# Kernel optimization log

Measured on AMD Instinct MI355X. Metric: run time of the kernel, lower is better.

Reference implementation:

```python
import jax, jax.numpy as jnp
import numpy as np

T, B = 200, 4096
CONTEXT_FRAMES = 6


def _lstm_cell(x, h, c, wih, whh, bih, bhh):
    # PyTorch LSTM gate order: i, f, g, o
    g = x @ wih.T + bih + h @ whh.T + bhh
    i, f, gg, o = jnp.split(g, 4, axis=-1)
    c2 = jax.nn.sigmoid(f) * c + jax.nn.sigmoid(i) * jnp.tanh(gg)
    h2 = jax.nn.sigmoid(o) * jnp.tanh(c2)
    return h2, c2


def _ff(x, w1, b1, w2, b2):
    return jax.nn.relu(jax.nn.relu(x @ w1.T + b1) @ w2.T + b2)


def setup_inputs() -> dict:
    key = jax.random.key(0)
    ks = iter(jax.random.split(key, 48))

    def p(shape, scale=0.1):
        return (jax.random.normal(next(ks), shape) * scale).astype(jnp.float32)

    inp = {
        'tactiles': p((T, B, 48), 1.0),
        'actions': p((T, B, 3), 1.0),
        'context': p((T, B, 48), 1.0),
    }
    # LSTM params: (4H, in), (4H, H), (4H,), (4H,)
    for name, din, h in [('l1', 48, 48), ('l2', 96, 96), ('l3', 144, 144), ('l4', 48, 48)]:
        inp[name + '_wih'] = p((4 * h, din))
        inp[name + '_whh'] = p((4 * h, h))
        inp[name + '_bih'] = p((4 * h,))
        inp[name + '_bhh'] = p((4 * h,))
    # Feedforward params
    for name, din, hid, dout in [('f1', 6, 48, 48), ('f2', 144, 144, 96), ('f3', 96, 96, 48)]:
        inp[name + '_w1'] = p((hid, din))
        inp[name + '_b1'] = p((hid,))
        inp[name + '_w2'] = p((dout, hid))
        inp[name + '_b2'] = p((dout,))
    # Hidden-state inits (original uses torch.rand -> uniform[0,1))
    for name, h in [('1', 48), ('2', 96), ('3', 144), ('4', 48)]:
        inp['h0_' + name] = jax.random.uniform(next(ks), (B, h), dtype=jnp.float32)
        inp['c0_' + name] = jax.random.uniform(next(ks), (B, h), dtype=jnp.float32)
    return inp


def reference(tactiles, actions, context,
              l1_wih, l1_whh, l1_bih, l1_bhh,
              l2_wih, l2_whh, l2_bih, l2_bhh,
              l3_wih, l3_whh, l3_bih, l3_bhh,
              l4_wih, l4_whh, l4_bih, l4_bhh,
              f1_w1, f1_b1, f1_w2, f1_b2,
              f2_w1, f2_b1, f2_w2, f2_b2,
              f3_w1, f3_b1, f3_w2, f3_b2,
              h0_1, c0_1, h0_2, c0_2, h0_3, c0_3, h0_4, c0_4):
    state = actions[0]  # [B, 3], fixed across time

    def step(carry, inp):
        h1, c1, h2, c2, h3, c3, h4, c4, out6 = carry
        tac, act, ctx, t = inp
        x1 = jnp.where(t > CONTEXT_FRAMES - 1, out6, tac)  # [B, 48]
        h1, c1 = _lstm_cell(x1, h1, c1, l1_wih, l1_whh, l1_bih, l1_bhh)
        x2 = jnp.concatenate([ctx, h1], axis=1)  # [B, 96]
        h2, c2 = _lstm_cell(x2, h2, c2, l2_wih, l2_whh, l2_bih, l2_bhh)
        sa = jnp.concatenate([state, act], axis=1)  # [B, 6]
        sa_out = _ff(sa, f1_w1, f1_b1, f1_w2, f1_b2)  # [B, 48]
        x3 = jnp.concatenate([sa_out, h2], axis=1)  # [B, 144]
        h3, c3 = _lstm_cell(x3, h3, c3, l3_wih, l3_whh, l3_bih, l3_bhh)
        out4 = _ff(h3, f2_w1, f2_b1, f2_w2, f2_b2)  # [B, 96]
        out5 = _ff(out4, f3_w1, f3_b1, f3_w2, f3_b2)  # [B, 48]
        h4, c4 = _lstm_cell(out5, h4, c4, l4_wih, l4_whh, l4_bih, l4_bhh)
        return (h1, c1, h2, c2, h3, c3, h4, c4, h4), h4

    carry0 = (h0_1, c0_1, h0_2, c0_2, h0_3, c0_3, h0_4, c0_4, jnp.zeros_like(h0_1))
    ts = jnp.arange(tactiles.shape[0])
    _, outs = jax.lax.scan(step, carry0, (tactiles, actions, context, ts))
    return outs  # [T, B, 48]
```

## Files before the change

kernel.cpp:

```cpp
#include <hip/hip_runtime.h>
#include <math.h>


#define NT 256
#define MROWS 8
#define TSTEPS 200
#define BATCH 4096
#define XS 10
#define GS 9

#define L1W   0
#define L1B   18432
#define L2W   18624
#define L2B   92352
#define L3W   92736
#define L3B   258624
#define L4W   259200
#define L4B   277632
#define F1AW  277824
#define F1AB  278208
#define F1BW  278256
#define F1BB  280560
#define F2AW  280608
#define F2AB  301344
#define F2BW  301488
#define F2BB  315312
#define F3AW  315408
#define F3AB  324624
#define F3BW  324720
#define F3BB  329328

#define P_GB   0
#define P_SAT  5184
#define P_F1H  5264
#define P_F2H  0
#define P_O4T  1440
#define P_F3H  2400
#define P_OUT5 3360
#define P_L4G  0
#define POOLSZ 5744

__device__ __forceinline__ float sigf(float x) { return 1.0f / (1.0f + __expf(-x)); }

__global__ void prep_lstm(const float* __restrict__ wih, const float* __restrict__ whh,
                          const float* __restrict__ bih, const float* __restrict__ bhh,
                          float* __restrict__ W, float* __restrict__ bias,
                          int Din, int H) {
    int K = Din + H;
    int N = 4 * H;
    int total = N * K;
    for (int idx = blockIdx.x * blockDim.x + threadIdx.x; idx < total + N;
         idx += gridDim.x * blockDim.x) {
        if (idx < total) {
            int c = idx / K;
            int k = idx - c * K;
            W[idx] = (k < Din) ? wih[c * Din + k] : whh[c * H + (k - Din)];
        } else {
            int c = idx - total;
            bias[c] = bih[c] + bhh[c];
        }
    }
}

__global__ void prep_ff(const float* __restrict__ w, const float* __restrict__ b,
                        float* __restrict__ W, float* __restrict__ bias,
                        int K, int Kpad, int N) {
    int total = N * Kpad;
    for (int idx = blockIdx.x * blockDim.x + threadIdx.x; idx < total + N;
         idx += gridDim.x * blockDim.x) {
        if (idx < total) {
            int c = idx / Kpad;
            int k = idx - c * Kpad;
            W[idx] = (k < K) ? w[c * K + k] : 0.0f;
        } else {
            int c = idx - total;
            bias[c] = b[c];
        }
    }
}

template <int TC, int ROWS, bool RELU>
__device__ __forceinline__ void mm(
    const float* __restrict__ w0, const float* __restrict__ w1,
    const float* __restrict__ w2,
    float b0, float b1, float b2,
    const float* __restrict__ x0, int K0,
    const float* __restrict__ x1, int K1,
    const float* __restrict__ x2, int K2,
    int rbase,
    float* __restrict__ g0, float* __restrict__ g1, float* __restrict__ g2) {
    float a0[ROWS], a1[ROWS], a2[ROWS];
#pragma unroll
    for (int r = 0; r < ROWS; ++r) { a0[r] = 0.f; a1[r] = 0.f; a2[r] = 0.f; }
    int ko = 0;
#pragma unroll
    for (int s = 0; s < 3; ++s) {
        const float* xb = (s == 0) ? x0 : (s == 1) ? x1 : x2;
        int K = (s == 0) ? K0 : (s == 1) ? K1 : K2;
        if (K > 0) {
            const float* xp = xb + rbase;
#pragma unroll 2
            for (int k = 0; k < K; k += 4) {
                float4 wv0 = *(const float4*)(w0 + ko + k);
                float4 wv1 = (TC > 1) ? *(const float4*)(w1 + ko + k) : wv0;
                float4 wv2 = (TC > 2) ? *(const float4*)(w2 + ko + k) : wv0;
                const float* f0 = (const float*)&wv0;
                const float* f1p = (const float*)&wv1;
                const float* f2p = (const float*)&wv2;
#pragma unroll
                for (int q = 0; q < 4; ++q) {
                    const float* xq = xp + (k + q) * XS;
#pragma unroll
                    for (int rr = 0; rr < ROWS; rr += 2) {
                        float2 xv = *(const float2*)(xq + rr);
                        a0[rr]     = fmaf(xv.x, f0[q], a0[rr]);
                        a0[rr + 1] = fmaf(xv.y, f0[q], a0[rr + 1]);
                        if (TC > 1) {
                            a1[rr]     = fmaf(xv.x, f1p[q], a1[rr]);
                            a1[rr + 1] = fmaf(xv.y, f1p[q], a1[rr + 1]);
                        }
                        if (TC > 2) {
                            a2[rr]     = fmaf(xv.x, f2p[q], a2[rr]);
                            a2[rr + 1] = fmaf(xv.y, f2p[q], a2[rr + 1]);
                        }
                    }
                }
            }
            ko += K;
        }
    }
#pragma unroll
    for (int r = 0; r < ROWS; ++r) {
        float v0 = a0[r] + b0;
        if (RELU) v0 = fmaxf(v0, 0.f);
        g0[r] = v0;
        if (TC > 1) {
            float v1 = a1[r] + b1;
            if (RELU) v1 = fmaxf(v1, 0.f);
            g1[r] = v1;
        }
        if (TC > 2) {
            float v2 = a2[r] + b2;
            if (RELU) v2 = fmaxf(v2, 0.f);
            g2[r] = v2;
        }
    }
}

template <int H, int R, int NCS>
__device__ __forceinline__ void lstm_epi(const float* __restrict__ gb, int gs,
                                         float* __restrict__ hT,
                                         float (&cs)[NCS], int idx0, int stride) {
    const int E = H * R;
#pragma unroll
    for (int n = 0; n < NCS; ++n) {
        int idx = idx0 + n * stride;
        if (idx < E) {
            int r = idx & (R - 1);
            int j = idx / R;
            float gi = gb[j * gs + r];
            float gf = gb[(j + H) * gs + r];
            float gg = gb[(j + 2 * H) * gs + r];
            float go = gb[(j + 3 * H) * gs + r];
            float c2 = sigf(gf) * cs[n] + sigf(gi) * tanhf(gg);
            cs[n] = c2;
            hT[j * XS + r] = sigf(go) * tanhf(c2);
        }
    }
}

template <int H, int R, int NCS>
__device__ __forceinline__ void c_init(const float* __restrict__ c0, int r0,
                                       float (&cs)[NCS], int idx0, int stride) {
    const int E = H * R;
#pragma unroll
    for (int n = 0; n < NCS; ++n) {
        int idx = idx0 + n * stride;
        if (idx < E) {
            int r = idx & (R - 1);
            int j = idx / R;
            cs[n] = c0[(size_t)(r0 + r) * H + j];
        }
    }
}

__global__ __launch_bounds__(256, 2) void model_kernel(
    const float* __restrict__ tactiles, const float* __restrict__ actions,
    const float* __restrict__ context, const float* __restrict__ ws,
    const float* __restrict__ h01, const float* __restrict__ c01,
    const float* __restrict__ h02, const float* __restrict__ c02,
    const float* __restrict__ h03, const float* __restrict__ c03,
    const float* __restrict__ h04, const float* __restrict__ c04,
    float* __restrict__ out) {
    __shared__ __align__(16) float tacT[48 * XS];
    __shared__ __align__(16) float ctxT[48 * XS];
    __shared__ __align__(16) float h1T[48 * XS];
    __shared__ __align__(16) float h2T[96 * XS];
    __shared__ __align__(16) float h3T[144 * XS];
    __shared__ __align__(16) float h4T[48 * XS];
    __shared__ __align__(16) float saoT[48 * XS];
    __shared__ __align__(16) float pool[POOLSZ];

    const int tid = threadIdx.x;
    const int r0 = blockIdx.x * MROWS;

    for (int i = tid; i < 48 * 8; i += NT) {
        int r = i & 7, j = i >> 3;
        h1T[j * XS + r] = h01[(size_t)(r0 + r) * 48 + j];
        h4T[j * XS + r] = h04[(size_t)(r0 + r) * 48 + j];
    }
    for (int i = tid; i < 96 * 8; i += NT) {
        int r = i & 7, j = i >> 3;
        h2T[j * XS + r] = h02[(size_t)(r0 + r) * 96 + j];
    }
    for (int i = tid; i < 144 * 8; i += NT) {
        int r = i & 7, j = i >> 3;
        h3T[j * XS + r] = h03[(size_t)(r0 + r) * 144 + j];
    }

    float cs1[2] = {0.f, 0.f};
    float cs2[3] = {0.f, 0.f, 0.f};
    float cs3[5] = {0.f, 0.f, 0.f, 0.f, 0.f};
    float cs4[2] = {0.f, 0.f};
    if (tid >= 64) c_init<48, 8, 2>(c01, r0, cs1, tid - 64, 192);
    c_init<96, 8, 3>(c02, r0, cs2, tid, NT);
    c_init<144, 8, 5>(c03, r0, cs3, tid, NT);
    c_init<48, 8, 2>(c04, r0, cs4, tid, NT);

    float bL1  = (tid < 192) ? ws[L1B + tid] : 0.f;
    float bL2a = ws[L2B + tid];
    float bL2b = (tid < 128) ? ws[L2B + tid + 256] : 0.f;
    float bL3a = ws[L3B + tid];
    float bL3b = ws[L3B + tid + 256];
    float bL3c = (tid < 64) ? ws[L3B + tid + 512] : 0.f;
    float bL4  = (tid < 192) ? ws[L4B + tid] : 0.f;
    float bF1a = (tid >= 192 && tid < 240) ? ws[F1AB + (tid - 192)] : 0.f;
    float bF1b = (tid < 48) ? ws[F1BB + tid] : 0.f;
    float bF2a = (tid < 144) ? ws[F2AB + tid] : 0.f;
    float bF2b = (tid < 192) ? ws[F2BB + (tid % 96)] : 0.f;
    float bF3a = (tid < 192) ? ws[F3AB + (tid % 96)] : 0.f;
    float bF3b = (tid < 192) ? ws[F3BB + (tid % 48)] : 0.f;

    const int wvid = tid >> 6;
    __syncthreads();

    for (int t = 0; t < TSTEPS; ++t) {
        if (t < 6) {
            const float* src = tactiles + (size_t)t * BATCH * 48 + (size_t)r0 * 48;
            for (int i = tid; i < 96; i += NT) {
                int r = i / 12, k4 = (i % 12) * 4;
                float4 v = *(const float4*)(src + r * 48 + k4);
                tacT[(k4 + 0) * XS + r] = v.x;
                tacT[(k4 + 1) * XS + r] = v.y;
                tacT[(k4 + 2) * XS + r] = v.z;
                tacT[(k4 + 3) * XS + r] = v.w;
            }
        }
        {
            const float* src = context + (size_t)t * BATCH * 48 + (size_t)r0 * 48;
            for (int i = tid; i < 96; i += NT) {
                int r = i / 12, k4 = (i % 12) * 4;
                float4 v = *(const float4*)(src + r * 48 + k4);
                ctxT[(k4 + 0) * XS + r] = v.x;
                ctxT[(k4 + 1) * XS + r] = v.y;
                ctxT[(k4 + 2) * XS + r] = v.z;
                ctxT[(k4 + 3) * XS + r] = v.w;
            }
        }
        if (tid < 64) {
            int r = tid & 7, k = tid >> 3;
            float v = 0.f;
            if (k < 3) v = actions[(size_t)(r0 + r) * 3 + k];
            else if (k < 6) v = actions[(size_t)t * BATCH * 3 + (size_t)(r0 + r) * 3 + (k - 3)];
            pool[P_SAT + k * XS + r] = v;
        }
        __syncthreads();

        {
            const float* x1 = (t < 6) ? tacT : h4T;
            if (tid < 192)
                mm<1, 8, false>(ws + L1W + tid * 96, ws, ws, bL1, 0.f, 0.f,
                                x1, 48, h1T, 48, nullptr, 0, 0,
                                pool + P_GB + tid * GS, nullptr, nullptr);
            else if (tid < 240)
                mm<1, 8, true>(ws + F1AW + (tid - 192) * 8, ws, ws, bF1a, 0.f, 0.f,
                               pool + P_SAT, 8, nullptr, 0, nullptr, 0, 0,
                               pool + P_F1H + (tid - 192) * XS, nullptr, nullptr);
        }
        __syncthreads();

        if (tid < 48)
            mm<1, 8, true>(ws + F1BW + tid * 48, ws, ws, bF1b, 0.f, 0.f,
                           pool + P_F1H, 48, nullptr, 0, nullptr, 0, 0,
                           saoT + tid * XS, nullptr, nullptr);
        else if (tid >= 64)
            lstm_epi<48, 8, 2>(pool + P_GB, GS, h1T, cs1, tid - 64, 192);
        __syncthreads();

        if (wvid < 2)
            mm<2, 8, false>(ws + L2W + (size_t)tid * 192, ws + L2W + (size_t)(tid + 256) * 192,
                            ws, bL2a, bL2b, 0.f,
                            ctxT, 48, h1T, 48, h2T, 96, 0,
                            pool + P_GB + tid * GS, pool + P_GB + (tid + 256) * GS, nullptr);
        else
            mm<1, 8, false>(ws + L2W + (size_t)tid * 192, ws, ws, bL2a, 0.f, 0.f,
                            ctxT, 48, h1T, 48, h2T, 96, 0,
                            pool + P_GB + tid * GS, nullptr, nullptr);
        __syncthreads();
        lstm_epi<96, 8, 3>(pool + P_GB, GS, h2T, cs2, tid, NT);
        __syncthreads();

        if (wvid == 0)
            mm<3, 8, false>(ws + L3W + (size_t)tid * 288, ws + L3W + (size_t)(tid + 256) * 288,
                            ws + L3W + (size_t)(tid + 512) * 288, bL3a, bL3b, bL3c,
                            saoT, 48, h2T, 96, h3T, 144, 0,
                            pool + P_GB + tid * GS, pool + P_GB + (tid + 256) * GS,
                            pool + P_GB + (tid + 512) * GS);
        else
            mm<2, 8, false>(ws + L3W + (size_t)tid * 288, ws + L3W + (size_t)(tid + 256) * 288,
                            ws, bL3a, bL3b, 0.f,
                            saoT, 48, h2T, 96, h3T, 144, 0,
                            pool + P_GB + tid * GS, pool + P_GB + (tid + 256) * GS, nullptr);
        __syncthreads();
        lstm_epi<144, 8, 5>(pool + P_GB, GS, h3T, cs3, tid, NT);
        __syncthreads();

        if (tid < 144)
            mm<1, 8, true>(ws + F2AW + tid * 144, ws, ws, bF2a, 0.f, 0.f,
                           h3T, 144, nullptr, 0, nullptr, 0, 0,
                           pool + P_F2H + tid * XS, nullptr, nullptr);
        __syncthreads();
        if (tid < 192) {
            int c = tid % 96, rb = (tid / 96) * 4;
            mm<1, 4, true>(ws + F2BW + c * 144, ws, ws, bF2b, 0.f, 0.f,
                           pool + P_F2H, 144, nullptr, 0, nullptr, 0, rb,
                           pool + P_O4T + c * XS + rb, nullptr, nullptr);
        }
        __syncthreads();
        if (tid < 192) {
            int c = tid % 96, rb = (tid / 96) * 4;
            mm<1, 4, true>(ws + F3AW + c * 96, ws, ws, bF3a, 0.f, 0.f,
                           pool + P_O4T, 96, nullptr, 0, nullptr, 0, rb,
                           pool + P_F3H + c * XS + rb, nullptr, nullptr);
        }
        __syncthreads();
        if (tid < 192) {
            int c = tid % 48, rb = (tid / 48) * 2;
            mm<1, 2, true>(ws + F3BW + c * 96, ws, ws, bF3b, 0.f, 0.f,
                           pool + P_F3H, 96, nullptr, 0, nullptr, 0, rb,
                           pool + P_OUT5 + c * XS + rb, nullptr, nullptr);
        }
        __syncthreads();

        if (tid < 192)
            mm<1, 8, false>(ws + L4W + tid * 96, ws, ws, bL4, 0.f, 0.f,
                            pool + P_OUT5, 48, h4T, 48, nullptr, 0, 0,
                            pool + P_L4G + tid * GS, nullptr, nullptr);
        __syncthreads();
        lstm_epi<48, 8, 2>(pool + P_L4G, GS, h4T, cs4, tid, NT);
        __syncthreads();

        {
            float* dst = out + (size_t)t * BATCH * 48 + (size_t)r0 * 48;
            for (int i = tid; i < 96; i += NT) {
                int r = i / 12, j4 = (i % 12) * 4;
                float4 v;
                v.x = h4T[(j4 + 0) * XS + r];
                v.y = h4T[(j4 + 1) * XS + r];
                v.z = h4T[(j4 + 2) * XS + r];
                v.w = h4T[(j4 + 3) * XS + r];
                *(float4*)(dst + r * 48 + j4) = v;
            }
        }
    }
}

extern "C" void kernel_launch(void* const* d_in, const int* in_sizes, int n_in,
                              void* d_out, int out_size, void* d_ws, size_t ws_size,
                              hipStream_t stream) {
    const float* tac = (const float*)d_in[0];
    const float* act = (const float*)d_in[1];
    const float* ctx = (const float*)d_in[2];

    const float* l1_wih = (const float*)d_in[3];
    const float* l1_whh = (const float*)d_in[4];
    const float* l1_bih = (const float*)d_in[5];
    const float* l1_bhh = (const float*)d_in[6];
    const float* l2_wih = (const float*)d_in[7];
    const float* l2_whh = (const float*)d_in[8];
    const float* l2_bih = (const float*)d_in[9];
    const float* l2_bhh = (const float*)d_in[10];
    const float* l3_wih = (const float*)d_in[11];
    const float* l3_whh = (const float*)d_in[12];
    const float* l3_bih = (const float*)d_in[13];
    const float* l3_bhh = (const float*)d_in[14];
    const float* l4_wih = (const float*)d_in[15];
    const float* l4_whh = (const float*)d_in[16];
    const float* l4_bih = (const float*)d_in[17];
    const float* l4_bhh = (const float*)d_in[18];

    const float* f1_w1 = (const float*)d_in[19];
    const float* f1_b1 = (const float*)d_in[20];
    const float* f1_w2 = (const float*)d_in[21];
    const float* f1_b2 = (const float*)d_in[22];
    const float* f2_w1 = (const float*)d_in[23];
    const float* f2_b1 = (const float*)d_in[24];
    const float* f2_w2 = (const float*)d_in[25];
    const float* f2_b2 = (const float*)d_in[26];
    const float* f3_w1 = (const float*)d_in[27];
    const float* f3_b1 = (const float*)d_in[28];
    const float* f3_w2 = (const float*)d_in[29];
    const float* f3_b2 = (const float*)d_in[30];

    const float* h01 = (const float*)d_in[31];
    const float* c01 = (const float*)d_in[32];
    const float* h02 = (const float*)d_in[33];
    const float* c02 = (const float*)d_in[34];
    const float* h03 = (const float*)d_in[35];
    const float* c03 = (const float*)d_in[36];
    const float* h04 = (const float*)d_in[37];
    const float* c04 = (const float*)d_in[38];

    float* ws = (float*)d_ws;
    float* out = (float*)d_out;

    dim3 blk(NT);
    hipLaunchKernelGGL(prep_lstm, dim3(96), blk, 0, stream,
                       l1_wih, l1_whh, l1_bih, l1_bhh, ws + L1W, ws + L1B, 48, 48);
    hipLaunchKernelGGL(prep_lstm, dim3(256), blk, 0, stream,
                       l2_wih, l2_whh, l2_bih, l2_bhh, ws + L2W, ws + L2B, 96, 96);
    hipLaunchKernelGGL(prep_lstm, dim3(256), blk, 0, stream,
                       l3_wih, l3_whh, l3_bih, l3_bhh, ws + L3W, ws + L3B, 144, 144);
    hipLaunchKernelGGL(prep_lstm, dim3(96), blk, 0, stream,
                       l4_wih, l4_whh, l4_bih, l4_bhh, ws + L4W, ws + L4B, 48, 48);

    hipLaunchKernelGGL(prep_ff, dim3(4), blk, 0, stream,
                       f1_w1, f1_b1, ws + F1AW, ws + F1AB, 6, 8, 48);
    hipLaunchKernelGGL(prep_ff, dim3(16), blk, 0, stream,
                       f1_w2, f1_b2, ws + F1BW, ws + F1BB, 48, 48, 48);
    hipLaunchKernelGGL(prep_ff, dim3(96), blk, 0, stream,
                       f2_w1, f2_b1, ws + F2AW, ws + F2AB, 144, 144, 144);
    hipLaunchKernelGGL(prep_ff, dim3(64), blk, 0, stream,
                       f2_w2, f2_b2, ws + F2BW, ws + F2BB, 144, 144, 96);
    hipLaunchKernelGGL(prep_ff, dim3(48), blk, 0, stream,
                       f3_w1, f3_b1, ws + F3AW, ws + F3AB, 96, 96, 96);
    hipLaunchKernelGGL(prep_ff, dim3(24), blk, 0, stream,
                       f3_w2, f3_b2, ws + F3BW, ws + F3BB, 96, 96, 48);

    hipLaunchKernelGGL(model_kernel, dim3(BATCH / MROWS), blk, 0, stream,
                       tac, act, ctx, ws,
                       h01, c01, h02, c02, h03, c03, h04, c04, out);
}
```

Baseline: 17.68 ms.

## Fuse LSTM gate matmul with cell epilogue via gate-interleaved weights and double-buffered state

```diff
diff --git a/kernel.cpp b/kernel.cpp
--- a/kernel.cpp
+++ b/kernel.cpp
@@ -6,7 +6,7 @@
 #define MROWS 8
 #define TSTEPS 200
 #define BATCH 4096
-#define XS 10
+#define XS 12
 #define GS 9
 
 #define L1W   0
@@ -31,16 +31,42 @@
 #define F3BB  329328
 
 #define P_GB   0
+#define P_F2H  0
+#define P_O4T  1728
+#define P_F3H  2880
+#define P_OUT5 4032
 #define P_SAT  5184
-#define P_F1H  5264
-#define P_F2H  0
-#define P_O4T  1440
-#define P_F3H  2400
-#define P_OUT5 3360
-#define P_L4G  0
-#define POOLSZ 5744
+#define P_F1H  5280
+#define POOLSZ 5856
+
+#define H1SZ (48 * XS)
+#define H2SZ (96 * XS)
+#define H4SZ (48 * XS)
 
 __device__ __forceinline__ float sigf(float x) { return 1.0f / (1.0f + __expf(-x)); }
+
+__global__ void prep_lstm_f(const float* __restrict__ wih, const float* __restrict__ whh,
+                            const float* __restrict__ bih, const float* __restrict__ bhh,
+                            float* __restrict__ W, float* __restrict__ bias,
+                            int Din, int H) {
+    int K = Din + H;
+    int total = H * K * 4;
+    for (int idx = blockIdx.x * blockDim.x + threadIdx.x; idx < total + 4 * H;
+         idx += gridDim.x * blockDim.x) {
+        if (idx < total) {
+            int g = idx & 3;
+            int kj = idx >> 2;
+            int k = kj % K;
+            int j = kj / K;
+            int row = g * H + j;
+            W[idx] = (k < Din) ? wih[row * Din + k] : whh[row * H + (k - Din)];
+        } else {
+            int i = idx - total;
+            int g = i & 3, j = i >> 2;
+            bias[i] = bih[g * H + j] + bhh[g * H + j];
+        }
+    }
+}
 
 __global__ void prep_lstm(const float* __restrict__ wih, const float* __restrict__ whh,
                           const float* __restrict__ bih, const float* __restrict__ bhh,
@@ -79,49 +105,158 @@
     }
 }
 
-template <int TC, int ROWS, bool RELU>
-__device__ __forceinline__ void mm(
+template <int ROWS, bool EMIT>
+__device__ __forceinline__ void lstm_fused(
+    const float* __restrict__ wp, float4 bv,
+    const float* __restrict__ x0, int K0,
+    const float* __restrict__ x1, int K1,
+    const float* __restrict__ x2, int K2,
+    int rbase, float* __restrict__ hdst,
+    float (&cs)[ROWS], float* __restrict__ gout) {
+    float ai[ROWS], af[ROWS], ag[ROWS], ao[ROWS];
+#pragma unroll
+    for (int r = 0; r < ROWS; ++r) { ai[r] = af[r] = ag[r] = ao[r] = 0.f; }
+    int ko = 0;
+#pragma unroll
+    for (int s = 0; s < 3; ++s) {
+        const float* xb = (s == 0) ? x0 : (s == 1) ? x1 : x2;
+        int K = (s == 0) ? K0 : (s == 1) ? K1 : K2;
+        if (K > 0) {
+            const float* xp = xb + rbase;
+            const float* wk = wp + (size_t)ko * 4;
+#pragma unroll 4
+            for (int k = 0; k < K; ++k) {
+                float4 wv = *(const float4*)(wk + k * 4);
+                if (ROWS == 2) {
+                    float2 xv = *(const float2*)(xp + k * XS);
+                    ai[0] = fmaf(xv.x, wv.x, ai[0]); ai[1] = fmaf(xv.y, wv.x, ai[1]);
+                    af[0] = fmaf(xv.x, wv.y, af[0]); af[1] = fmaf(xv.y, wv.y, af[1]);
+                    ag[0] = fmaf(xv.x, wv.z, ag[0]); ag[1] = fmaf(xv.y, wv.z, ag[1]);
+                    ao[0] = fmaf(xv.x, wv.w, ao[0]); ao[1] = fmaf(xv.y, wv.w, ao[1]);
+                } else {
+                    float4 xv = *(const float4*)(xp + k * XS);
+                    const float* xf = (const float*)&xv;
+#pragma unroll
+                    for (int r = 0; r < ROWS; ++r) {
+                        ai[r] = fmaf(xf[r], wv.x, ai[r]);
+                        af[r] = fmaf(xf[r], wv.y, af[r]);
+                        ag[r] = fmaf(xf[r], wv.z, ag[r]);
+                        ao[r] = fmaf(xf[r], wv.w, ao[r]);
+                    }
+                }
+            }
+            ko += K;
+        }
+    }
+    float hv[ROWS];
+#pragma unroll
+    for (int r = 0; r < ROWS; ++r) {
+        float gi = sigf(ai[r] + bv.x);
+        float gf = sigf(af[r] + bv.y);
+        float gg = tanhf(ag[r] + bv.z);
+        float go = sigf(ao[r] + bv.w);
+        float c2 = gf * cs[r] + gi * gg;
+        cs[r] = c2;
+        hv[r] = go * tanhf(c2);
+    }
+    if (ROWS == 2) {
+        *(float2*)hdst = make_float2(hv[0], hv[1]);
+    } else {
+        *(float4*)hdst = make_float4(hv[0], hv[1], hv[2], hv[3]);
+    }
+    if (EMIT) {
+#pragma unroll
+        for (int r = 0; r < ROWS; ++r) gout[(size_t)r * 48] = hv[r];
+    }
+}
+
+template <int ROWS>
+__device__ __forceinline__ void ffmm(
+    const float* __restrict__ w, float b,
+    const float* __restrict__ x, int K,
+    int rbase, float* __restrict__ dst) {
+    float a[ROWS];
+#pragma unroll
+    for (int r = 0; r < ROWS; ++r) a[r] = 0.f;
+    const float* xp = x + rbase;
+#pragma unroll 2
+    for (int k = 0; k < K; k += 4) {
+        float4 wv = *(const float4*)(w + k);
+        const float* wf = (const float*)&wv;
+#pragma unroll
+        for (int q = 0; q < 4; ++q) {
+            const float* xq = xp + (k + q) * XS;
+            if (ROWS == 8) {
+                float4 u = *(const float4*)(xq);
+                float4 v = *(const float4*)(xq + 4);
+                a[0] = fmaf(u.x, wf[q], a[0]); a[1] = fmaf(u.y, wf[q], a[1]);
+                a[2] = fmaf(u.z, wf[q], a[2]); a[3] = fmaf(u.w, wf[q], a[3]);
+                a[4] = fmaf(v.x, wf[q], a[4]); a[5] = fmaf(v.y, wf[q], a[5]);
+                a[6] = fmaf(v.z, wf[q], a[6]); a[7] = fmaf(v.w, wf[q], a[7]);
+            } else if (ROWS == 4) {
+                float4 u = *(const float4*)(xq);
+                a[0] = fmaf(u.x, wf[q], a[0]); a[1] = fmaf(u.y, wf[q], a[1]);
+                a[2] = fmaf(u.z, wf[q], a[2]); a[3] = fmaf(u.w, wf[q], a[3]);
+            } else {
+                float2 u = *(const float2*)(xq);
+                a[0] = fmaf(u.x, wf[q], a[0]); a[1] = fmaf(u.y, wf[q], a[1]);
+            }
+        }
+    }
+#pragma unroll
+    for (int r = 0; r < ROWS; ++r) a[r] = fmaxf(a[r] + b, 0.f);
+    if (ROWS == 8) {
+        *(float4*)(dst) = make_float4(a[0], a[1], a[2], a[3]);
+        *(float4*)(dst + 4) = make_float4(a[4], a[5], a[6], a[7]);
+    } else if (ROWS == 4) {
+        *(float4*)(dst) = make_float4(a[0], a[1], a[2], a[3]);
+    } else {
+        *(float2*)(dst) = make_float2(a[0], a[1]);
+    }
+}
+
+template <int TC>
+__device__ __forceinline__ void l3mm(
     const float* __restrict__ w0, const float* __restrict__ w1,
     const float* __restrict__ w2,
     float b0, float b1, float b2,
     const float* __restrict__ x0, int K0,
     const float* __restrict__ x1, int K1,
     const float* __restrict__ x2, int K2,
-    int rbase,
     float* __restrict__ g0, float* __restrict__ g1, float* __restrict__ g2) {
-    float a0[ROWS], a1[ROWS], a2[ROWS];
-#pragma unroll
-    for (int r = 0; r < ROWS; ++r) { a0[r] = 0.f; a1[r] = 0.f; a2[r] = 0.f; }
+    float a0[8], a1[8], a2[8];
+#pragma unroll
+    for (int r = 0; r < 8; ++r) { a0[r] = 0.f; a1[r] = 0.f; a2[r] = 0.f; }
     int ko = 0;
 #pragma unroll
     for (int s = 0; s < 3; ++s) {
         const float* xb = (s == 0) ? x0 : (s == 1) ? x1 : x2;
         int K = (s == 0) ? K0 : (s == 1) ? K1 : K2;
         if (K > 0) {
-            const float* xp = xb + rbase;
 #pragma unroll 2
             for (int k = 0; k < K; k += 4) {
                 float4 wv0 = *(const float4*)(w0 + ko + k);
-                float4 wv1 = (TC > 1) ? *(const float4*)(w1 + ko + k) : wv0;
+                float4 wv1 = *(const float4*)(w1 + ko + k);
                 float4 wv2 = (TC > 2) ? *(const float4*)(w2 + ko + k) : wv0;
                 const float* f0 = (const float*)&wv0;
                 const float* f1p = (const float*)&wv1;
                 const float* f2p = (const float*)&wv2;
 #pragma unroll
                 for (int q = 0; q < 4; ++q) {
-                    const float* xq = xp + (k + q) * XS;
-#pragma unroll
-                    for (int rr = 0; rr < ROWS; rr += 2) {
-                        float2 xv = *(const float2*)(xq + rr);
-                        a0[rr]     = fmaf(xv.x, f0[q], a0[rr]);
-                        a0[rr + 1] = fmaf(xv.y, f0[q], a0[rr + 1]);
-                        if (TC > 1) {
-                            a1[rr]     = fmaf(xv.x, f1p[q], a1[rr]);
-                            a1[rr + 1] = fmaf(xv.y, f1p[q], a1[rr + 1]);
-                        }
+                    const float* xq = xb + (k + q) * XS;
+                    float4 u = *(const float4*)(xq);
+                    float4 v = *(const float4*)(xq + 4);
+                    const float* xf = (const float*)&u;
+                    const float* yf = (const float*)&v;
+#pragma unroll
+                    for (int r = 0; r < 4; ++r) {
+                        a0[r] = fmaf(xf[r], f0[q], a0[r]);
+                        a0[r + 4] = fmaf(yf[r], f0[q], a0[r + 4]);
+                        a1[r] = fmaf(xf[r], f1p[q], a1[r]);
+                        a1[r + 4] = fmaf(yf[r], f1p[q], a1[r + 4]);
                         if (TC > 2) {
-                            a2[rr]     = fmaf(xv.x, f2p[q], a2[rr]);
-                            a2[rr + 1] = fmaf(xv.y, f2p[q], a2[rr + 1]);
+                            a2[r] = fmaf(xf[r], f2p[q], a2[r]);
+                            a2[r + 4] = fmaf(yf[r], f2p[q], a2[r + 4]);
                         }
                     }
                 }
@@ -130,20 +265,10 @@
         }
     }
 #pragma unroll
-    for (int r = 0; r < ROWS; ++r) {
-        float v0 = a0[r] + b0;
-        if (RELU) v0 = fmaxf(v0, 0.f);
-        g0[r] = v0;
-        if (TC > 1) {
-            float v1 = a1[r] + b1;
-            if (RELU) v1 = fmaxf(v1, 0.f);
-            g1[r] = v1;
-        }
-        if (TC > 2) {
-            float v2 = a2[r] + b2;
-            if (RELU) v2 = fmaxf(v2, 0.f);
-            g2[r] = v2;
-        }
+    for (int r = 0; r < 8; ++r) {
+        g0[r] = a0[r] + b0;
+        g1[r] = a1[r] + b1;
+        if (TC > 2) g2[r] = a2[r] + b2;
     }
 }
 
@@ -184,6 +309,14 @@
     }
 }
 
+template <int ROWS>
+__device__ __forceinline__ void c_init_f(const float* __restrict__ c0, int H,
+                                         int r0, int rbase, int j, float (&cs)[ROWS]) {
+#pragma unroll
+    for (int i = 0; i < ROWS; ++i)
+        cs[i] = c0[(size_t)(r0 + rbase + i) * H + j];
+}
+
 __global__ __launch_bounds__(256, 2) void model_kernel(
     const float* __restrict__ tactiles, const float* __restrict__ actions,
     const float* __restrict__ context, const float* __restrict__ ws,
@@ -194,11 +327,11 @@
     float* __restrict__ out) {
     __shared__ __align__(16) float tacT[48 * XS];
     __shared__ __align__(16) float ctxT[48 * XS];
-    __shared__ __align__(16) float h1T[48 * XS];
-    __shared__ __align__(16) float h2T[96 * XS];
+    __shared__ __align__(16) float saoT[48 * XS];
+    __shared__ __align__(16) float h1T[2 * H1SZ];
+    __shared__ __align__(16) float h2T[2 * H2SZ];
     __shared__ __align__(16) float h3T[144 * XS];
-    __shared__ __align__(16) float h4T[48 * XS];
-    __shared__ __align__(16) float saoT[48 * XS];
+    __shared__ __align__(16) float h4T[2 * H4SZ];
     __shared__ __align__(16) float pool[POOLSZ];
 
     const int tid = threadIdx.x;
@@ -206,12 +339,12 @@
 
     for (int i = tid; i < 48 * 8; i += NT) {
         int r = i & 7, j = i >> 3;
-        h1T[j * XS + r] = h01[(size_t)(r0 + r) * 48 + j];
-        h4T[j * XS + r] = h04[(size_t)(r0 + r) * 48 + j];
+        h1T[H1SZ + j * XS + r] = h01[(size_t)(r0 + r) * 48 + j];
+        h4T[H4SZ + j * XS + r] = h04[(size_t)(r0 + r) * 48 + j];
     }
     for (int i = tid; i < 96 * 8; i += NT) {
         int r = i & 7, j = i >> 3;
-        h2T[j * XS + r] = h02[(size_t)(r0 + r) * 96 + j];
+        h2T[H2SZ + j * XS + r] = h02[(size_t)(r0 + r) * 96 + j];
     }
     for (int i = tid; i < 144 * 8; i += NT) {
         int r = i & 7, j = i >> 3;
@@ -219,159 +352,169 @@
     }
 
     float cs1[2] = {0.f, 0.f};
-    float cs2[3] = {0.f, 0.f, 0.f};
+    float cs2[4] = {0.f, 0.f, 0.f, 0.f};
     float cs3[5] = {0.f, 0.f, 0.f, 0.f, 0.f};
     float cs4[2] = {0.f, 0.f};
-    if (tid >= 64) c_init<48, 8, 2>(c01, r0, cs1, tid - 64, 192);
-    c_init<96, 8, 3>(c02, r0, cs2, tid, NT);
+    if (tid < 192) {
+        c_init_f<2>(c01, 48, r0, (tid & 3) * 2, tid >> 2, cs1);
+        c_init_f<4>(c02, 96, r0, (tid & 1) * 4, tid >> 1, cs2);
+        c_init_f<2>(c04, 48, r0, (tid & 3) * 2, tid >> 2, cs4);
+    }
     c_init<144, 8, 5>(c03, r0, cs3, tid, NT);
-    c_init<48, 8, 2>(c04, r0, cs4, tid, NT);
-
-    float bL1  = (tid < 192) ? ws[L1B + tid] : 0.f;
-    float bL2a = ws[L2B + tid];
-    float bL2b = (tid < 128) ? ws[L2B + tid + 256] : 0.f;
+
+    float4 bL1v = make_float4(0.f, 0.f, 0.f, 0.f), bL2v = bL1v, bL4v = bL1v;
+    if (tid < 192) {
+        bL1v = *(const float4*)(ws + L1B + (tid >> 2) * 4);
+        bL2v = *(const float4*)(ws + L2B + (tid >> 1) * 4);
+        bL4v = *(const float4*)(ws + L4B + (tid >> 2) * 4);
+    }
     float bL3a = ws[L3B + tid];
     float bL3b = ws[L3B + tid + 256];
     float bL3c = (tid < 64) ? ws[L3B + tid + 512] : 0.f;
-    float bL4  = (tid < 192) ? ws[L4B + tid] : 0.f;
     float bF1a = (tid >= 192 && tid < 240) ? ws[F1AB + (tid - 192)] : 0.f;
-    float bF1b = (tid < 48) ? ws[F1BB + tid] : 0.f;
+    float bF1b = (tid >= 192 && tid < 240) ? ws[F1BB + (tid - 192)] : 0.f;
     float bF2a = (tid < 144) ? ws[F2AB + tid] : 0.f;
     float bF2b = (tid < 192) ? ws[F2BB + (tid % 96)] : 0.f;
     float bF3a = (tid < 192) ? ws[F3AB + (tid % 96)] : 0.f;
     float bF3b = (tid < 192) ? ws[F3BB + (tid % 48)] : 0.f;
 
     const int wvid = tid >> 6;
-    __syncthreads();
-
-    for (int t = 0; t < TSTEPS; ++t) {
-        if (t < 6) {
-            const float* src = tactiles + (size_t)t * BATCH * 48 + (size_t)r0 * 48;
-            for (int i = tid; i < 96; i += NT) {
-                int r = i / 12, k4 = (i % 12) * 4;
-                float4 v = *(const float4*)(src + r * 48 + k4);
-                tacT[(k4 + 0) * XS + r] = v.x;
-                tacT[(k4 + 1) * XS + r] = v.y;
-                tacT[(k4 + 2) * XS + r] = v.z;
-                tacT[(k4 + 3) * XS + r] = v.w;
-            }
-        }
-        {
-            const float* src = context + (size_t)t * BATCH * 48 + (size_t)r0 * 48;
-            for (int i = tid; i < 96; i += NT) {
-                int r = i / 12, k4 = (i % 12) * 4;
-                float4 v = *(const float4*)(src + r * 48 + k4);
-                ctxT[(k4 + 0) * XS + r] = v.x;
-                ctxT[(k4 + 1) * XS + r] = v.y;
-                ctxT[(k4 + 2) * XS + r] = v.z;
-                ctxT[(k4 + 3) * XS + r] = v.w;
-            }
+
+    {
+        const float* src = tactiles + (size_t)r0 * 48;
+        for (int i = tid; i < 96; i += NT) {
+            int r = i / 12, k4 = (i % 12) * 4;
+            float4 v = *(const float4*)(src + r * 48 + k4);
+            tacT[(k4 + 0) * XS + r] = v.x;
+            tacT[(k4 + 1) * XS + r] = v.y;
+            tacT[(k4 + 2) * XS + r] = v.z;
+            tacT[(k4 + 3) * XS + r] = v.w;
+        }
+        const float* csrc = context + (size_t)r0 * 48;
+        for (int i = tid; i < 96; i += NT) {
+            int r = i / 12, k4 = (i % 12) * 4;
+            float4 v = *(const float4*)(csrc + r * 48 + k4);
+            ctxT[(k4 + 0) * XS + r] = v.x;
+            ctxT[(k4 + 1) * XS + r] = v.y;
+            ctxT[(k4 + 2) * XS + r] = v.z;
+            ctxT[(k4 + 3) * XS + r] = v.w;
         }
         if (tid < 64) {
             int r = tid & 7, k = tid >> 3;
             float v = 0.f;
             if (k < 3) v = actions[(size_t)(r0 + r) * 3 + k];
-            else if (k < 6) v = actions[(size_t)t * BATCH * 3 + (size_t)(r0 + r) * 3 + (k - 3)];
+            else if (k < 6) v = actions[(size_t)(r0 + r) * 3 + (k - 3)];
             pool[P_SAT + k * XS + r] = v;
         }
-        __syncthreads();
-
-        {
-            const float* x1 = (t < 6) ? tacT : h4T;
-            if (tid < 192)
-                mm<1, 8, false>(ws + L1W + tid * 96, ws, ws, bL1, 0.f, 0.f,
-                                x1, 48, h1T, 48, nullptr, 0, 0,
-                                pool + P_GB + tid * GS, nullptr, nullptr);
-            else if (tid < 240)
-                mm<1, 8, true>(ws + F1AW + (tid - 192) * 8, ws, ws, bF1a, 0.f, 0.f,
-                               pool + P_SAT, 8, nullptr, 0, nullptr, 0, 0,
-                               pool + P_F1H + (tid - 192) * XS, nullptr, nullptr);
-        }
-        __syncthreads();
-
-        if (tid < 48)
-            mm<1, 8, true>(ws + F1BW + tid * 48, ws, ws, bF1b, 0.f, 0.f,
-                           pool + P_F1H, 48, nullptr, 0, nullptr, 0, 0,
-                           saoT + tid * XS, nullptr, nullptr);
-        else if (tid >= 64)
-            lstm_epi<48, 8, 2>(pool + P_GB, GS, h1T, cs1, tid - 64, 192);
-        __syncthreads();
-
-        if (wvid < 2)
-            mm<2, 8, false>(ws + L2W + (size_t)tid * 192, ws + L2W + (size_t)(tid + 256) * 192,
-                            ws, bL2a, bL2b, 0.f,
-                            ctxT, 48, h1T, 48, h2T, 96, 0,
-                            pool + P_GB + tid * GS, pool + P_GB + (tid + 256) * GS, nullptr);
+    }
+    __syncthreads();
+
+    for (int t = 0; t < TSTEPS; ++t) {
+        const int cur = t & 1, prev = cur ^ 1;
+
+        if (tid < 192) {
+            int j = tid >> 2, rg = tid & 3;
+            const float* x1src = (t < 6) ? tacT : (h4T + prev * H4SZ);
+            lstm_fused<2, false>(ws + L1W + (size_t)j * 96 * 4, bL1v,
+                                 x1src, 48, h1T + prev * H1SZ, 48, nullptr, 0,
+                                 rg * 2, h1T + cur * H1SZ + j * XS + rg * 2,
+                                 cs1, nullptr);
+        } else if (tid < 240) {
+            ffmm<8>(ws + F1AW + (tid - 192) * 8, bF1a, pool + P_SAT, 8, 0,
+                    pool + P_F1H + (tid - 192) * XS);
+        }
+        __syncthreads();
+
+        if (tid < 192) {
+            int j = tid >> 1, rg = tid & 1;
+            lstm_fused<4, false>(ws + L2W + (size_t)j * 192 * 4, bL2v,
+                                 ctxT, 48, h1T + cur * H1SZ, 48, h2T + prev * H2SZ, 96,
+                                 rg * 4, h2T + cur * H2SZ + j * XS + rg * 4,
+                                 cs2, nullptr);
+        } else if (tid < 240) {
+            ffmm<8>(ws + F1BW + (tid - 192) * 48, bF1b, pool + P_F1H, 48, 0,
+                    saoT + (tid - 192) * XS);
+        }
+        __syncthreads();
+
+        if (wvid == 0)
+            l3mm<3>(ws + L3W + (size_t)tid * 288, ws + L3W + (size_t)(tid + 256) * 288,
+                    ws + L3W + (size_t)(tid + 512) * 288, bL3a, bL3b, bL3c,
+                    saoT, 48, h2T + cur * H2SZ, 96, h3T, 144,
+                    pool + P_GB + tid * GS, pool + P_GB + (tid + 256) * GS,
+                    pool + P_GB + (tid + 512) * GS);
         else
-            mm<1, 8, false>(ws + L2W + (size_t)tid * 192, ws, ws, bL2a, 0.f, 0.f,
-                            ctxT, 48, h1T, 48, h2T, 96, 0,
-                            pool + P_GB + tid * GS, nullptr, nullptr);
-        __syncthreads();
-        lstm_epi<96, 8, 3>(pool + P_GB, GS, h2T, cs2, tid, NT);
-        __syncthreads();
-
-        if (wvid == 0)
-            mm<3, 8, false>(ws + L3W + (size_t)tid * 288, ws + L3W + (size_t)(tid + 256) * 288,
-                            ws + L3W + (size_t)(tid + 512) * 288, bL3a, bL3b, bL3c,
-                            saoT, 48, h2T, 96, h3T, 144, 0,
-                            pool + P_GB + tid * GS, pool + P_GB + (tid + 256) * GS,
-                            pool + P_GB + (tid + 512) * GS);
-        else
-            mm<2, 8, false>(ws + L3W + (size_t)tid * 288, ws + L3W + (size_t)(tid + 256) * 288,
-                            ws, bL3a, bL3b, 0.f,
-                            saoT, 48, h2T, 96, h3T, 144, 0,
-                            pool + P_GB + tid * GS, pool + P_GB + (tid + 256) * GS, nullptr);
+            l3mm<2>(ws + L3W + (size_t)tid * 288, ws + L3W + (size_t)(tid + 256) * 288,
+                    ws, bL3a, bL3b, 0.f,
+                    saoT, 48, h2T + cur * H2SZ, 96, h3T, 144,
+                    pool + P_GB + tid * GS, pool + P_GB + (tid + 256) * GS, nullptr);
         __syncthreads();
         lstm_epi<144, 8, 5>(pool + P_GB, GS, h3T, cs3, tid, NT);
         __syncthreads();
 
         if (tid < 144)
-            mm<1, 8, true>(ws + F2AW + tid * 144, ws, ws, bF2a, 0.f, 0.f,
-                           h3T, 144, nullptr, 0, nullptr, 0, 0,
-                           pool + P_F2H + tid * XS, nullptr, nullptr);
+            ffmm<8>(ws + F2AW + tid * 144, bF2a, h3T, 144, 0,
+                    pool + P_F2H + tid * XS);
         __syncthreads();
         if (tid < 192) {
             int c = tid % 96, rb = (tid / 96) * 4;
-            mm<1, 4, true>(ws + F2BW + c * 144, ws, ws, bF2b, 0.f, 0.f,
-                           pool + P_F2H, 144, nullptr, 0, nullptr, 0, rb,
-                           pool + P_O4T + c * XS + rb, nullptr, nullptr);
+            ffmm<4>(ws + F2BW + c * 144, bF2b, pool + P_F2H, 144, rb,
+                    pool + P_O4T + c * XS + rb);
         }
         __syncthreads();
         if (tid < 192) {
             int c = tid % 96, rb = (tid / 96) * 4;
-            mm<1, 4, true>(ws + F3AW + c * 96, ws, ws, bF3a, 0.f, 0.f,
-                           pool + P_O4T, 96, nullptr, 0, nullptr, 0, rb,
-                           pool + P_F3H + c * XS + rb, nullptr, nullptr);
+            ffmm<4>(ws + F3AW + c * 96, bF3a, pool + P_O4T, 96, rb,
+                    pool + P_F3H + c * XS + rb);
         }
         __syncthreads();
         if (tid < 192) {
             int c = tid % 48, rb = (tid / 48) * 2;
-            mm<1, 2, true>(ws + F3BW + c * 96, ws, ws, bF3b, 0.f, 0.f,
-                           pool + P_F3H, 96, nullptr, 0, nullptr, 0, rb,
-                           pool + P_OUT5 + c * XS + rb, nullptr, nullptr);
-        }
-        __syncthreads();
-
-        if (tid < 192)
-            mm<1, 8, false>(ws + L4W + tid * 96, ws, ws, bL4, 0.f, 0.f,
-                            pool + P_OUT5, 48, h4T, 48, nullptr, 0, 0,
-                            pool + P_L4G + tid * GS, nullptr, nullptr);
-        __syncthreads();
-        lstm_epi<48, 8, 2>(pool + P_L4G, GS, h4T, cs4, tid, NT);
-        __syncthreads();
-
-        {
-            float* dst = out + (size_t)t * BATCH * 48 + (size_t)r0 * 48;
-            for (int i = tid; i < 96; i += NT) {
-                int r = i / 12, j4 = (i % 12) * 4;
-                float4 v;
-                v.x = h4T[(j4 + 0) * XS + r];
-                v.y = h4T[(j4 + 1) * XS + r];
-                v.z = h4T[(j4 + 2) * XS + r];
-                v.w = h4T[(j4 + 3) * XS + r];
-                *(float4*)(dst + r * 48 + j4) = v;
+            ffmm<2>(ws + F3BW + c * 96, bF3b, pool + P_F3H, 96, rb,
+                    pool + P_OUT5 + c * XS + rb);
+        }
+        __syncthreads();
+
+        if (tid < 192) {
+            int j = tid >> 2, rg = tid & 3;
+            float* gout = out + (size_t)t * (BATCH * 48) + (size_t)(r0 + rg * 2) * 48 + j;
+            lstm_fused<2, true>(ws + L4W + (size_t)j * 96 * 4, bL4v,
+                                pool + P_OUT5, 48, h4T + prev * H4SZ, 48, nullptr, 0,
+                                rg * 2, h4T + cur * H4SZ + j * XS + rg * 2,
+                                cs4, gout);
+        } else if (t + 1 < TSTEPS) {
+            int i2 = tid - 192;
+            if (t + 1 < 6) {
+                const float* src = tactiles + (size_t)(t + 1) * (BATCH * 48) + (size_t)r0 * 48;
+                for (int i = i2; i < 96; i += 64) {
+                    int r = i / 12, k4 = (i % 12) * 4;
+                    float4 v = *(const float4*)(src + r * 48 + k4);
+                    tacT[(k4 + 0) * XS + r] = v.x;
+                    tacT[(k4 + 1) * XS + r] = v.y;
+                    tacT[(k4 + 2) * XS + r] = v.z;
+                    tacT[(k4 + 3) * XS + r] = v.w;
+                }
             }
-        }
+            {
+                const float* src = context + (size_t)(t + 1) * (BATCH * 48) + (size_t)r0 * 48;
+                for (int i = i2; i < 96; i += 64) {
+                    int r = i / 12, k4 = (i % 12) * 4;
+                    float4 v = *(const float4*)(src + r * 48 + k4);
+                    ctxT[(k4 + 0) * XS + r] = v.x;
+                    ctxT[(k4 + 1) * XS + r] = v.y;
+                    ctxT[(k4 + 2) * XS + r] = v.z;
+                    ctxT[(k4 + 3) * XS + r] = v.w;
+                }
+            }
+            {
+                int r = i2 & 7, k = i2 >> 3;
+                float v = 0.f;
+                if (k < 3) v = actions[(size_t)(r0 + r) * 3 + k];
+                else if (k < 6) v = actions[(size_t)(t + 1) * (BATCH * 3) + (size_t)(r0 + r) * 3 + (k - 3)];
+                pool[P_SAT + k * XS + r] = v;
+            }
+        }
+        __syncthreads();
     }
 }
 
@@ -425,13 +568,13 @@
     float* out = (float*)d_out;
 
     dim3 blk(NT);
-    hipLaunchKernelGGL(prep_lstm, dim3(96), blk, 0, stream,
+    hipLaunchKernelGGL(prep_lstm_f, dim3(96), blk, 0, stream,
                        l1_wih, l1_whh, l1_bih, l1_bhh, ws + L1W, ws + L1B, 48, 48);
-    hipLaunchKernelGGL(prep_lstm, dim3(256), blk, 0, stream,
+    hipLaunchKernelGGL(prep_lstm_f, dim3(256), blk, 0, stream,
                        l2_wih, l2_whh, l2_bih, l2_bhh, ws + L2W, ws + L2B, 96, 96);
     hipLaunchKernelGGL(prep_lstm, dim3(256), blk, 0, stream,
                        l3_wih, l3_whh, l3_bih, l3_bhh, ws + L3W, ws + L3B, 144, 144);
-    hipLaunchKernelGGL(prep_lstm, dim3(96), blk, 0, stream,
+    hipLaunchKernelGGL(prep_lstm_f, dim3(96), blk, 0, stream,
                        l4_wih, l4_whh, l4_bih, l4_bhh, ws + L4W, ws + L4B, 48, 48);
 
     hipLaunchKernelGGL(prep_ff, dim3(4), blk, 0, stream,
```

Measured after the change: 16.78 ms. 5.1% less time.
